# Performance work log

Measured on AMD Instinct MI355X. Metric: run time of the kernel, lower is better.

The kernel has to match this reference:

```python
import jax, jax.numpy as jnp
import numpy as np
import math

T, B, E, H = 256, 128, 1024, 1024


def setup_inputs() -> dict:
    key = jax.random.key(0)
    ks = jax.random.split(key, 5)
    bound = 1.0 / math.sqrt(H)
    u = lambda k: jax.random.uniform(k, (H, H + E), jnp.float32, -bound, bound)
    return {
        "embeds": jax.random.normal(ks[0], (T, B, E), jnp.float32),
        "W_g": u(ks[1]),
        "W_i": u(ks[2]),
        "W_f": u(ks[3]),
        "W_o": u(ks[4]),
        "b_g": jnp.zeros((H,), jnp.float32),
        "b_i": jnp.zeros((H,), jnp.float32),
        "b_f": jnp.ones((H,), jnp.float32),
        "b_o": jnp.zeros((H,), jnp.float32),
    }


def reference(embeds, W_g, W_i, W_f, W_o, b_g, b_i, b_f, b_o):
    Tn, Bn, _ = embeds.shape
    Hn = W_g.shape[0]
    # Fuse the 4 gate GEMMs into one: rows are concatenated -> identical math.
    W = jnp.concatenate([W_g, W_i, W_f, W_o], axis=0)      # (4H, H+E)
    b = jnp.concatenate([b_g, b_i, b_f, b_o], axis=0)      # (4H,)

    def step(carry, x_t):
        h_prev, c_prev = carry
        xh = jnp.concatenate([x_t, h_prev], axis=1)         # (B, E+H)
        z = xh @ W.T + b                                    # (B, 4H)
        g = jnp.tanh(z[:, :Hn])
        i = jax.nn.sigmoid(z[:, Hn:2 * Hn])
        f = jax.nn.sigmoid(z[:, 2 * Hn:3 * Hn])
        o = jax.nn.sigmoid(z[:, 3 * Hn:])
        c_t = f * c_prev + i * g
        h_t = o * jnp.tanh(c_t)
        return (h_t, c_t), h_t

    h0 = jnp.zeros((Bn, Hn), embeds.dtype)
    c0 = jnp.zeros((Bn, Hn), embeds.dtype)
    # Original loop starts at t=1 (embeds[0] unused, output[0] = zeros).
    _, hs = jax.lax.scan(step, (h0, c0), embeds[1:])
    return jnp.concatenate([h0[None], hs], axis=0)          # (T, B, H)
```

## Files before the change

### kernel.cpp

```cpp
#include <hip/hip_runtime.h>
#include <cstdint>
#include <cstddef>

#define Tn 256
#define Bn 128
#define En 1024
#define Hn 1024
#define NG 4096

typedef __bf16 bf16;
typedef __bf16 bf16x8 __attribute__((ext_vector_type(8)));
typedef __bf16 bf16x4 __attribute__((ext_vector_type(4)));
typedef float  f32x4  __attribute__((ext_vector_type(4)));
typedef float  f32x2  __attribute__((ext_vector_type(2)));

typedef __attribute__((address_space(1))) void gvoid;
typedef __attribute__((address_space(3))) void lvoid;

__device__ __forceinline__ float sigmoidf_(float x) {
  return 1.0f / (1.0f + __expf(-x));
}

__device__ __forceinline__ float bf16_of(unsigned w, int j) {
  unsigned short s = (j == 0) ? (unsigned short)(w & 0xffffu)
                              : (unsigned short)(w >> 16);
  return (float)__builtin_bit_cast(bf16, s);
}

__global__ __launch_bounds__(256) void prep_w(
    const float* __restrict__ Wg, const float* __restrict__ Wi,
    const float* __restrict__ Wf, const float* __restrict__ Wo,
    const float* __restrict__ bg, const float* __restrict__ bi,
    const float* __restrict__ bff, const float* __restrict__ bo,
    bf16* __restrict__ Wx, bf16* __restrict__ Wh, float* __restrict__ bias)
{
  int idx = blockIdx.x * 256 + threadIdx.x;
  int g = idx >> 20;
  int r = idx & 0xFFFFF;
  int u = r >> 10;
  int k = r & 1023;
  const float* Ws = (g == 0) ? Wg : (g == 1) ? Wi : (g == 2) ? Wf : Wo;
  size_t src = (size_t)u * (En + Hn) + k;
  Wx[idx] = (bf16)Ws[src];
  Wh[idx] = (bf16)Ws[src + En];
  if (idx < NG) {
    int gg = idx >> 10, uu = idx & 1023;
    const float* bs = (gg == 0) ? bg : (gg == 1) ? bi : (gg == 2) ? bff : bo;
    bias[idx] = bs[uu];
  }
}

__global__ __launch_bounds__(256) void conv_x(const float* __restrict__ X,
                                              bf16* __restrict__ Xb)
{
  int idx = blockIdx.x * 256 + threadIdx.x;
  f32x4 v = ((const f32x4*)X)[idx];
  bf16x4 o;
  o[0] = (bf16)v[0]; o[1] = (bf16)v[1]; o[2] = (bf16)v[2]; o[3] = (bf16)v[3];
  ((bf16x4*)Xb)[idx] = o;
}

__global__ __launch_bounds__(256) void zx_gemm(
    const bf16* __restrict__ Xb, const bf16* __restrict__ Wx,
    const float* __restrict__ bias, bf16* __restrict__ zx)
{
  const int tid  = threadIdx.x;
  const int lane = tid & 63;
  const int w    = tid >> 6;
  const int l15  = lane & 15;
  const int lq   = lane >> 4;
  const int wm   = w >> 1, wn = w & 1;

  const int n0 = blockIdx.x * 128;
  const int m0 = blockIdx.y * 128;

  __shared__ bf16 As[128 * 32];
  __shared__ bf16 Bs[128 * 32];

  const f32x4 zero4 = {0.f, 0.f, 0.f, 0.f};
  f32x4 acc[4][4];
  #pragma unroll
  for (int i = 0; i < 4; ++i)
    #pragma unroll
    for (int j = 0; j < 4; ++j) acc[i][j] = zero4;

  const int srow = w * 32 + (lane >> 2);
  const int scol = (lane & 3) * 8;
  const bf16* Asrc = Xb + ((size_t)(128 + m0 + srow)) * En + scol;
  const bf16* Bsrc = Wx + ((size_t)(n0 + srow)) * En + scol;
  bf16* Adst0 = &As[(w * 32 +  0) * 32];
  bf16* Adst1 = &As[(w * 32 + 16) * 32];
  bf16* Bdst0 = &Bs[(w * 32 +  0) * 32];
  bf16* Bdst1 = &Bs[(w * 32 + 16) * 32];

  for (int kc = 0; kc < En / 32; ++kc) {
    __builtin_amdgcn_global_load_lds((const gvoid*)(Asrc + kc * 32),
                                     (lvoid*)Adst0, 16, 0, 0);
    __builtin_amdgcn_global_load_lds((const gvoid*)(Asrc + (size_t)16 * En + kc * 32),
                                     (lvoid*)Adst1, 16, 0, 0);
    __builtin_amdgcn_global_load_lds((const gvoid*)(Bsrc + kc * 32),
                                     (lvoid*)Bdst0, 16, 0, 0);
    __builtin_amdgcn_global_load_lds((const gvoid*)(Bsrc + (size_t)16 * En + kc * 32),
                                     (lvoid*)Bdst1, 16, 0, 0);
    __syncthreads();

    bf16x8 a[4], b[4];
    #pragma unroll
    for (int i = 0; i < 4; ++i)
      a[i] = *(const bf16x8*)&As[(wm * 64 + i * 16 + l15) * 32 + lq * 8];
    #pragma unroll
    for (int j = 0; j < 4; ++j)
      b[j] = *(const bf16x8*)&Bs[(wn * 64 + j * 16 + l15) * 32 + lq * 8];

    #pragma unroll
    for (int i = 0; i < 4; ++i)
      #pragma unroll
      for (int j = 0; j < 4; ++j)
        acc[i][j] = __builtin_amdgcn_mfma_f32_16x16x32_bf16(a[i], b[j],
                                                            acc[i][j], 0, 0, 0);
    __syncthreads();
  }

  #pragma unroll
  for (int i = 0; i < 4; ++i)
    #pragma unroll
    for (int j = 0; j < 4; ++j)
      #pragma unroll
      for (int r = 0; r < 4; ++r) {
        int m = m0 + wm * 64 + i * 16 + lq * 4 + r;
        int n = n0 + wn * 64 + j * 16 + l15;
        zx[(size_t)m * NG + n] = (bf16)(acc[i][j][r] + bias[n]);
      }
}

#define HS_STRIDE 1032

__global__ __launch_bounds__(256, 1) void lstm_persist(
    const bf16* __restrict__ Wh,
    const bf16* __restrict__ zx,
    bf16* __restrict__ hb0,
    bf16* __restrict__ hb1,
    float* __restrict__ out,
    unsigned int* __restrict__ flags)
{
  const int tid  = threadIdx.x;
  const int lane = tid & 63;
  const int g    = tid >> 6;
  const int l15  = lane & 15;
  const int lq   = lane >> 4;
  const int ut   = blockIdx.x & 63;
  const int qb   = blockIdx.x >> 6;

  __shared__ bf16  hs[32 * HS_STRIDE];
  __shared__ float zs[4][32][18];

  bf16x8 wfrag[32];
  {
    const bf16* wp = Wh + ((size_t)(g * Hn + ut * 16 + l15)) * Hn + lq * 8;
    #pragma unroll
    for (int ks = 0; ks < 32; ++ks)
      wfrag[ks] = *(const bf16x8*)(wp + ks * 32);
  }

  const int bl   = tid >> 3;
  const int up0  = (tid & 7) << 1;
  const int brow = qb * 32 + bl;
  const int u0   = ut * 16 + up0;

  float creg[2] = {0.f, 0.f};
  const f32x4 zero4 = {0.f, 0.f, 0.f, 0.f};

  for (int t = 1; t < Tn; ++t) {
    const bf16* hin  = ((t - 1) & 1) ? hb1 : hb0;
    bf16*       hout = (t & 1) ? hb1 : hb0;

    unsigned zxw[4];
    {
      const bf16* zrow = zx + ((size_t)(t - 1) * Bn + brow) * NG + u0;
      #pragma unroll
      for (int gg = 0; gg < 4; ++gg)
        zxw[gg] = *(const unsigned*)(zrow + gg * Hn);
    }

    if (t > 1) {
      unsigned int* fp = flags + (((size_t)(t - 1)) * 4 + (size_t)qb) * 64;
      for (;;) {
        unsigned v = __hip_atomic_load(&fp[lane], __ATOMIC_RELAXED,
                                       __HIP_MEMORY_SCOPE_AGENT);
        if (__ballot(v != 0u) == ~0ULL) break;
        __builtin_amdgcn_s_sleep(1);
      }
    }

    #pragma unroll
    for (int j = 0; j < 16; ++j) {
      int rh   = g * 16 + j;
      int row  = rh >> 1;
      int half = rh & 1;
      const bf16* src = hin + ((size_t)(qb * 32 + row)) * Hn + half * 512 + lane * 8;
      bf16* dst = &hs[row * HS_STRIDE + half * 512];
      __builtin_amdgcn_global_load_lds((const gvoid*)src, (lvoid*)dst, 16, 0, 0x11);
    }
    __syncthreads();

    f32x4 acc[2] = {zero4, zero4};
    #pragma unroll
    for (int ks = 0; ks < 32; ++ks) {
      bf16x8 a0 = *(const bf16x8*)&hs[(l15) * HS_STRIDE + ks * 32 + lq * 8];
      bf16x8 a1 = *(const bf16x8*)&hs[(16 + l15) * HS_STRIDE + ks * 32 + lq * 8];
      acc[0] = __builtin_amdgcn_mfma_f32_16x16x32_bf16(a0, wfrag[ks], acc[0], 0, 0, 0);
      acc[1] = __builtin_amdgcn_mfma_f32_16x16x32_bf16(a1, wfrag[ks], acc[1], 0, 0, 0);
    }

    #pragma unroll
    for (int mt = 0; mt < 2; ++mt)
      #pragma unroll
      for (int i = 0; i < 4; ++i)
        zs[g][mt * 16 + lq * 4 + i][l15] = acc[mt][i];
    __syncthreads();

    float hv0, hv1;
    {
      float hv[2];
      unsigned short hp[2];
      #pragma unroll
      for (int j = 0; j < 2; ++j) {
        int ul = up0 + j;
        float zg = zs[0][bl][ul] + bf16_of(zxw[0], j);
        float zi = zs[1][bl][ul] + bf16_of(zxw[1], j);
        float zf = zs[2][bl][ul] + bf16_of(zxw[2], j);
        float zo = zs[3][bl][ul] + bf16_of(zxw[3], j);
        float gv = tanhf(zg);
        float iv = sigmoidf_(zi);
        float fv = sigmoidf_(zf);
        float ov = sigmoidf_(zo);
        float cv = fv * creg[j] + iv * gv;
        creg[j] = cv;
        hv[j] = ov * tanhf(cv);
        hp[j] = __builtin_bit_cast(unsigned short, (bf16)hv[j]);
      }
      size_t off = (size_t)brow * Hn + u0;
      unsigned hpack = (unsigned)hp[0] | ((unsigned)hp[1] << 16);
      __hip_atomic_store((unsigned int*)(hout + off), hpack,
                         __ATOMIC_RELAXED, __HIP_MEMORY_SCOPE_AGENT);
      hv0 = hv[0]; hv1 = hv[1];
    }

    asm volatile("s_waitcnt vmcnt(0)" ::: "memory");
    __syncthreads();
    if (t < Tn - 1 && tid == 0) {
      __hip_atomic_store(&flags[((size_t)t * 4 + (size_t)qb) * 64 + ut], 1u,
                         __ATOMIC_RELAXED, __HIP_MEMORY_SCOPE_AGENT);
    }

    {
      size_t off = (size_t)brow * Hn + u0;
      f32x2 ov2 = {hv0, hv1};
      __builtin_nontemporal_store(ov2, (f32x2*)(out + (size_t)t * Bn * Hn + off));
    }
  }
}

extern "C" void kernel_launch(void* const* d_in, const int* in_sizes, int n_in,
                              void* d_out, int out_size, void* d_ws, size_t ws_size,
                              hipStream_t stream) {
  const float* embeds = (const float*)d_in[0];
  const float* Wg = (const float*)d_in[1];
  const float* Wi = (const float*)d_in[2];
  const float* Wf = (const float*)d_in[3];
  const float* Wo = (const float*)d_in[4];
  const float* bg = (const float*)d_in[5];
  const float* bi = (const float*)d_in[6];
  const float* bff = (const float*)d_in[7];
  const float* bo = (const float*)d_in[8];
  float* out = (float*)d_out;

  char* ws = (char*)d_ws;
  bf16*  Wx   = (bf16*)(ws + 0);
  bf16*  Wh   = (bf16*)(ws + 8388608);
  float* bias = (float*)(ws + 16777216);
  bf16*  Xb   = (bf16*)(ws + 16793600);
  bf16*  zx   = (bf16*)(ws + 83902464);
  bf16*  h0b  = (bf16*)(ws + 351289344);
  bf16*  h1b  = (bf16*)(ws + 351551488);
  unsigned int* flags = (unsigned int*)(ws + 0);

  hipMemsetAsync(out, 0, (size_t)Bn * Hn * sizeof(float), stream);
  hipMemsetAsync(h0b, 0, (size_t)Bn * Hn * sizeof(bf16), stream);

  prep_w<<<16384, 256, 0, stream>>>(Wg, Wi, Wf, Wo, bg, bi, bff, bo, Wx, Wh, bias);
  conv_x<<<32768, 256, 0, stream>>>(embeds, Xb);
  zx_gemm<<<dim3(32, 255), 256, 0, stream>>>(Xb, Wx, bias, zx);

  hipMemsetAsync(flags, 0, (size_t)256 * 4 * 64 * sizeof(unsigned int), stream);

  void* args[] = {(void*)&Wh, (void*)&zx, (void*)&h0b, (void*)&h1b,
                  (void*)&out, (void*)&flags};
  hipLaunchCooperativeKernel((void*)lstm_persist, dim3(256), dim3(256),
                             args, 0, stream);
}
```

Before: 1.942 ms.

## Split recurrent GEMM over K across waves and reduce partial gate sums in LDS

```diff
diff --git a/kernel.cpp b/kernel.cpp
--- a/kernel.cpp
+++ b/kernel.cpp
@@ -145,21 +145,23 @@
 {
   const int tid  = threadIdx.x;
   const int lane = tid & 63;
-  const int g    = tid >> 6;
+  const int kq   = tid >> 6;
   const int l15  = lane & 15;
   const int lq   = lane >> 4;
   const int ut   = blockIdx.x & 63;
   const int qb   = blockIdx.x >> 6;
 
   __shared__ bf16  hs[32 * HS_STRIDE];
-  __shared__ float zs[4][32][18];
-
-  bf16x8 wfrag[32];
-  {
-    const bf16* wp = Wh + ((size_t)(g * Hn + ut * 16 + l15)) * Hn + lq * 8;
-    #pragma unroll
-    for (int ks = 0; ks < 32; ++ks)
-      wfrag[ks] = *(const bf16x8*)(wp + ks * 32);
+  __shared__ float zs[4][4][32][18];
+
+  bf16x8 wfrag[4][8];
+  #pragma unroll
+  for (int g = 0; g < 4; ++g) {
+    const bf16* wp = Wh + ((size_t)(g * Hn + ut * 16 + l15)) * Hn
+                        + kq * 256 + lq * 8;
+    #pragma unroll
+    for (int ks = 0; ks < 8; ++ks)
+      wfrag[g][ks] = *(const bf16x8*)(wp + ks * 32);
   }
 
   const int bl   = tid >> 3;
@@ -194,7 +196,7 @@
 
     #pragma unroll
     for (int j = 0; j < 16; ++j) {
-      int rh   = g * 16 + j;
+      int rh   = kq * 16 + j;
       int row  = rh >> 1;
       int half = rh & 1;
       const bf16* src = hin + ((size_t)(qb * 32 + row)) * Hn + half * 512 + lane * 8;
@@ -203,33 +205,56 @@
     }
     __syncthreads();
 
-    f32x4 acc[2] = {zero4, zero4};
-    #pragma unroll
-    for (int ks = 0; ks < 32; ++ks) {
-      bf16x8 a0 = *(const bf16x8*)&hs[(l15) * HS_STRIDE + ks * 32 + lq * 8];
-      bf16x8 a1 = *(const bf16x8*)&hs[(16 + l15) * HS_STRIDE + ks * 32 + lq * 8];
-      acc[0] = __builtin_amdgcn_mfma_f32_16x16x32_bf16(a0, wfrag[ks], acc[0], 0, 0, 0);
-      acc[1] = __builtin_amdgcn_mfma_f32_16x16x32_bf16(a1, wfrag[ks], acc[1], 0, 0, 0);
-    }
-
+    f32x4 acc[2][4];
     #pragma unroll
     for (int mt = 0; mt < 2; ++mt)
       #pragma unroll
-      for (int i = 0; i < 4; ++i)
-        zs[g][mt * 16 + lq * 4 + i][l15] = acc[mt][i];
+      for (int g = 0; g < 4; ++g) acc[mt][g] = zero4;
+
+    #pragma unroll
+    for (int ks = 0; ks < 8; ++ks) {
+      bf16x8 a0 = *(const bf16x8*)&hs[(l15) * HS_STRIDE + kq * 256 + ks * 32 + lq * 8];
+      bf16x8 a1 = *(const bf16x8*)&hs[(16 + l15) * HS_STRIDE + kq * 256 + ks * 32 + lq * 8];
+      #pragma unroll
+      for (int g = 0; g < 4; ++g) {
+        acc[0][g] = __builtin_amdgcn_mfma_f32_16x16x32_bf16(a0, wfrag[g][ks],
+                                                            acc[0][g], 0, 0, 0);
+        acc[1][g] = __builtin_amdgcn_mfma_f32_16x16x32_bf16(a1, wfrag[g][ks],
+                                                            acc[1][g], 0, 0, 0);
+      }
+    }
+
+    #pragma unroll
+    for (int g = 0; g < 4; ++g)
+      #pragma unroll
+      for (int mt = 0; mt < 2; ++mt)
+        #pragma unroll
+        for (int i = 0; i < 4; ++i)
+          zs[kq][g][mt * 16 + lq * 4 + i][l15] = acc[mt][g][i];
     __syncthreads();
 
     float hv0, hv1;
     {
+      float zsum[4][2];
+      #pragma unroll
+      for (int g = 0; g < 4; ++g) { zsum[g][0] = 0.f; zsum[g][1] = 0.f; }
+      #pragma unroll
+      for (int kk = 0; kk < 4; ++kk)
+        #pragma unroll
+        for (int g = 0; g < 4; ++g) {
+          f32x2 v = *(const f32x2*)&zs[kk][g][bl][up0];
+          zsum[g][0] += v[0];
+          zsum[g][1] += v[1];
+        }
+
       float hv[2];
       unsigned short hp[2];
       #pragma unroll
       for (int j = 0; j < 2; ++j) {
-        int ul = up0 + j;
-        float zg = zs[0][bl][ul] + bf16_of(zxw[0], j);
-        float zi = zs[1][bl][ul] + bf16_of(zxw[1], j);
-        float zf = zs[2][bl][ul] + bf16_of(zxw[2], j);
-        float zo = zs[3][bl][ul] + bf16_of(zxw[3], j);
+        float zg = zsum[0][j] + bf16_of(zxw[0], j);
+        float zi = zsum[1][j] + bf16_of(zxw[1], j);
+        float zf = zsum[2][j] + bf16_of(zxw[2], j);
+        float zo = zsum[3][j] + bf16_of(zxw[3], j);
         float gv = tanhf(zg);
         float iv = sigmoidf_(zi);
         float fv = sigmoidf_(zf);
```

New measurement: 1.880 ms. -3.2%, faster.
